# Optimization experiments

Measured on AMD Instinct MI355X. Metric: run time of the kernel, lower is better.

## Reference

```python
import jax, jax.numpy as jnp
import numpy as np

N_NODES = 50000
N_EDGES = 800000
N_POS = 200000
NFEAT = 512
NHID = 256


def setup_inputs() -> dict:
    key = jax.random.key(0)
    ks = jax.random.split(key, 7)
    x = jax.random.normal(ks[0], (N_NODES, NFEAT), dtype=jnp.float32)
    edge_index = jax.random.randint(ks[1], (2, N_EDGES), 0, N_NODES, dtype=jnp.int32)
    edge_weight = jax.random.uniform(ks[2], (N_EDGES,), dtype=jnp.float32)
    pos_edge_index = jax.random.randint(ks[3], (2, N_POS), 0, N_NODES, dtype=jnp.int32)
    W1 = jax.random.normal(ks[4], (NFEAT, NHID), dtype=jnp.float32) * (1.0 / np.sqrt(NFEAT))
    W2 = jax.random.normal(ks[5], (NHID, NHID), dtype=jnp.float32) * (1.0 / np.sqrt(NHID))
    Wlin = jax.random.normal(ks[6], (2 * NHID, 2), dtype=jnp.float32) * (1.0 / np.sqrt(2 * NHID))
    return {"x": x, "edge_index": edge_index, "edge_weight": edge_weight,
            "pos_edge_index": pos_edge_index, "W1": W1, "W2": W2, "Wlin": Wlin}


def _gcn_conv(h, W, src, dst, edge_weight, num_nodes):
    # GCNConv(normalize=False, add_self_loops=False, bias=False):
    # out[dst] += edge_weight * (h @ W)[src]
    h = h @ W  # [N, out]
    msg = edge_weight[:, None] * h[src]  # [E, out]
    return jax.ops.segment_sum(msg, dst, num_segments=num_nodes)


def reference(x, edge_index, edge_weight, pos_edge_index, W1, W2, Wlin):
    src, dst = edge_index[0], edge_index[1]
    n = x.shape[0]
    z = _gcn_conv(x, W1, src, dst, edge_weight, n)
    z = jax.nn.relu(z)
    z = _gcn_conv(z, W2, src, dst, edge_weight, n)
    # decode: gather endpoints, concat, linear (no bias)
    h = jnp.concatenate([z[pos_edge_index[0]], z[pos_edge_index[1]]], axis=1)  # [P, 2*nhid]
    return h @ Wlin  # [P, 2]
```

## Files before the change

### kernel.cpp

```cpp
#include <hip/hip_runtime.h>

#define NHID 256
#define NFEAT 512

using short8  = __attribute__((ext_vector_type(8))) short;
using float8  = __attribute__((ext_vector_type(8))) float;
using f32x4   = __attribute__((ext_vector_type(4))) float;

__device__ __forceinline__ float b2f(unsigned short u) {
    union { float f; unsigned v; } c;
    c.v = ((unsigned)u) << 16;
    return c.f;
}
__device__ __forceinline__ unsigned short f2b(float f) {
    union { float f; unsigned u; } c;
    c.f = f;
    unsigned r = c.u + 0x7fffu + ((c.u >> 16) & 1u);
    return (unsigned short)(r >> 16);
}
__device__ __forceinline__ unsigned short f2h(float f) {
    union { _Float16 h; unsigned short u; } c;
    c.h = (_Float16)f;
    return c.u;
}
__device__ __forceinline__ float h2f(unsigned short u) {
    union { _Float16 h; unsigned short u; } c;
    c.u = u;
    return (float)c.h;
}

__device__ __forceinline__ void gload16(const void* gsrc, void* lds) {
    __builtin_amdgcn_global_load_lds((const __attribute__((address_space(1))) unsigned int*)gsrc,
                                     (__attribute__((address_space(3))) unsigned int*)lds,
                                     16, 0, 0);
}

__global__ __launch_bounds__(256) void prep_all(const float* __restrict__ W1,
                                                const float* __restrict__ W2,
                                                const float* __restrict__ Wlin,
                                                unsigned short* __restrict__ F1,
                                                float* __restrict__ WP,
                                                int* __restrict__ cursor, int M) {
    int i = blockIdx.x * blockDim.x + threadIdx.x;
    const int T1 = NFEAT * NHID;
    if (i < T1) {
        int j = i & 7, l = (i >> 3) & 63, cb = (i >> 9) & 15, t = i >> 13;
        int n = cb * 16 + (l & 15);
        int k = t * 32 + ((l >> 4) << 3) + j;
        F1[i] = f2b(W1[k * NHID + n]);
    } else if (i < T1 + NHID * 4) {
        int i3 = i - T1;
        int k = i3 >> 2, j = i3 & 3;
        const int base = (j >= 2) ? NHID : 0;
        const int col = j & 1;
        float acc = 0.f;
        for (int n = 0; n < NHID; ++n)
            acc += W2[k * NHID + n] * Wlin[(base + n) * 2 + col];
        WP[k * 4 + j] = acc;
    } else {
        int j = i - T1 - NHID * 4;
        if (j < M) cursor[j] = 0;
    }
}

__device__ __forceinline__ void gemm1_body(const float* __restrict__ x,
                                           const unsigned short* __restrict__ F1,
                                           unsigned short* __restrict__ C, int M,
                                           int brow, char* AsRaw ) {
    const int tid = threadIdx.x;
    const int lane = tid & 63;
    const int wc = tid >> 6;
    const int lrow = lane & 15;
    const int lq = lane >> 4;
    const int nt = NFEAT / 32;

    int ar0 = brow + wc * 16 + (lane >> 3);
    int ar1 = ar0 + 8;
    if (ar0 >= M) ar0 = M - 1;
    if (ar1 >= M) ar1 = M - 1;
    const int aswz = ((lane & 7) ^ (lane >> 3)) * 4;
    const float* ag0 = x + (size_t)ar0 * NFEAT + aswz;
    const float* ag1 = x + (size_t)ar1 * NFEAT + aswz;
    const unsigned short* bsrc = F1 + (wc * 4) * 512 + lane * 8;

    f32x4 acc[4][4] = {};

    gload16(ag0, AsRaw + wc * 2048);
    gload16(ag1, AsRaw + wc * 2048 + 1024);
    short8 bc0 = *(const short8*)(bsrc + 0 * 512);
    short8 bc1 = *(const short8*)(bsrc + 1 * 512);
    short8 bc2 = *(const short8*)(bsrc + 2 * 512);
    short8 bc3 = *(const short8*)(bsrc + 3 * 512);
    __syncthreads();

    int p = 0;
#pragma unroll
    for (int t = 0; t < 16; ++t) {
        short8 bn0, bn1, bn2, bn3;
        if (t + 1 < nt) {
            gload16(ag0 + (t + 1) * 32, AsRaw + (p ^ 1) * 8192 + wc * 2048);
            gload16(ag1 + (t + 1) * 32, AsRaw + (p ^ 1) * 8192 + wc * 2048 + 1024);
            const unsigned short* bs_ = bsrc + (t + 1) * 8192;
            bn0 = *(const short8*)(bs_ + 0 * 512);
            bn1 = *(const short8*)(bs_ + 1 * 512);
            bn2 = *(const short8*)(bs_ + 2 * 512);
            bn3 = *(const short8*)(bs_ + 3 * 512);
        }
        short8 a[4];
#pragma unroll
        for (int m = 0; m < 4; ++m) {
            int row = m * 16 + lrow;
            const char* base = AsRaw + p * 8192 + row * 128;
            int sw = (row & 7) << 4;
            float4 f0 = *(const float4*)(base + ((lq * 32) ^ sw));
            float4 f1 = *(const float4*)(base + ((lq * 32 + 16) ^ sw));
            short8 v;
            v[0] = (short)f2b(f0.x); v[1] = (short)f2b(f0.y);
            v[2] = (short)f2b(f0.z); v[3] = (short)f2b(f0.w);
            v[4] = (short)f2b(f1.x); v[5] = (short)f2b(f1.y);
            v[6] = (short)f2b(f1.z); v[7] = (short)f2b(f1.w);
            a[m] = v;
        }
#pragma unroll
        for (int m = 0; m < 4; ++m) {
            acc[m][0] = __builtin_amdgcn_mfma_f32_16x16x32_bf16(a[m], bc0, acc[m][0], 0, 0, 0);
            acc[m][1] = __builtin_amdgcn_mfma_f32_16x16x32_bf16(a[m], bc1, acc[m][1], 0, 0, 0);
            acc[m][2] = __builtin_amdgcn_mfma_f32_16x16x32_bf16(a[m], bc2, acc[m][2], 0, 0, 0);
            acc[m][3] = __builtin_amdgcn_mfma_f32_16x16x32_bf16(a[m], bc3, acc[m][3], 0, 0, 0);
        }
        __syncthreads();
        p ^= 1;
        bc0 = bn0; bc1 = bn1; bc2 = bn2; bc3 = bn3;
    }

#pragma unroll
    for (int m = 0; m < 4; ++m)
#pragma unroll
        for (int r = 0; r < 4; ++r) {
            int row = brow + m * 16 + (lane >> 4) * 4 + r;
            if (row < M) {
#pragma unroll
                for (int n = 0; n < 4; ++n) {
                    int col = wc * 64 + n * 16 + (lane & 15);
                    C[(size_t)row * NHID + col] = f2b(acc[m][n][r]);
                }
            }
        }
}

__global__ __launch_bounds__(256) void fused_g1_histrank(const float* __restrict__ x,
                                                         const unsigned short* __restrict__ F1,
                                                         unsigned short* __restrict__ C, int M,
                                                         int gblocks,
                                                         const int* __restrict__ dst,
                                                         int* __restrict__ counts,
                                                         int* __restrict__ rank, int E) {
    __shared__ char AsRaw[2 * 8192];
    if ((int)blockIdx.x < gblocks) {
        gemm1_body(x, F1, C, M, blockIdx.x * 64, AsRaw);
    } else {
        const int rank_b = blockIdx.x - gblocks;
        const int nrank = gridDim.x - gblocks;
        for (int e = rank_b * blockDim.x + threadIdx.x; e < E; e += nrank * blockDim.x)
            rank[e] = atomicAdd(&counts[dst[e]], 1);
    }
}

__global__ __launch_bounds__(256) void fused_g1_ranksort(const float* __restrict__ x,
                                                         const unsigned short* __restrict__ F1,
                                                         unsigned short* __restrict__ C, int M,
                                                         int gblocks, int rowbase,
                                                         const int* __restrict__ src,
                                                         const int* __restrict__ dst,
                                                         const float* __restrict__ w,
                                                         const int* __restrict__ offsets,
                                                         const int* __restrict__ rank,
                                                         unsigned* __restrict__ pk,
                                                         int E, int span) {
    __shared__ char AsRaw[2 * 8192];
    if ((int)blockIdx.x < gblocks) {
        gemm1_body(x, F1, C, M, (rowbase + blockIdx.x) * 64, AsRaw);
    } else {
        const int rb = blockIdx.x - gblocks;
        const int nrb = gridDim.x - gblocks;
        const int g = rb & 7;
        const int r8 = rb >> 3;
        const int n8 = nrb >> 3;
        const int lo = g * span;
        const int hi = min(lo + span, M);
        for (int e = r8 * blockDim.x + threadIdx.x; e < E; e += n8 * blockDim.x) {
            int d = dst[e];
            if (d >= lo && d < hi)
                pk[offsets[d] + rank[e]] = ((unsigned)f2h(w[e]) << 16) | (unsigned)src[e];
        }
    }
}

__global__ __launch_bounds__(1024) void scan_local(const int* __restrict__ counts,
                                                   int* __restrict__ local,
                                                   int* __restrict__ blocksums, int n) {
    __shared__ int s[1024];
    const int tid = threadIdx.x;
    const int idx = blockIdx.x * 1024 + tid;
    int v = (idx < n) ? counts[idx] : 0;
    s[tid] = v;
    __syncthreads();
    for (int off = 1; off < 1024; off <<= 1) {
        int t = (tid >= off) ? s[tid - off] : 0;
        __syncthreads();
        s[tid] += t;
        __syncthreads();
    }
    if (idx < n) local[idx] = s[tid] - v;
    if (tid == 1023) blocksums[blockIdx.x] = s[1023];
}

__global__ __launch_bounds__(1024) void scan_sums(int* __restrict__ blocksums, int nb) {
    __shared__ int s[1024];
    const int tid = threadIdx.x;
    int v = (tid < nb) ? blocksums[tid] : 0;
    s[tid] = v;
    __syncthreads();
    for (int off = 1; off < 1024; off <<= 1) {
        int t = (tid >= off) ? s[tid - off] : 0;
        __syncthreads();
        s[tid] += t;
        __syncthreads();
    }
    if (tid < nb) blocksums[tid] = s[tid] - v;
}

__global__ __launch_bounds__(256) void scan_finalize(int* __restrict__ offsets,
                                                     const int* __restrict__ blockoffs,
                                                     int n, int total) {
    int idx = blockIdx.x * blockDim.x + threadIdx.x;
    if (idx < n) offsets[idx] += blockoffs[idx >> 10];
    if (idx == 0) offsets[n] = total;
}

__global__ __launch_bounds__(256) void gather1_proj(const unsigned short* __restrict__ h,
                                                    const int* __restrict__ offsets,
                                                    const unsigned* __restrict__ pk,
                                                    const float* __restrict__ WP,
                                                    float4* __restrict__ y4, int N) {
    const int lane = threadIdx.x & 63;
    const int wid = threadIdx.x >> 6;
    const int node = blockIdx.x * 4 + wid;
    if (node >= N) return;

    float wp[4][4];
#pragma unroll
    for (int i = 0; i < 4; ++i) {
        float4 r = ((const float4*)WP)[lane * 4 + i];
        wp[i][0] = r.x; wp[i][1] = r.y; wp[i][2] = r.z; wp[i][3] = r.w;
    }

    const int s0 = offsets[node];
    const int s1 = offsets[node + 1];
    float a0 = 0.f, a1 = 0.f, a2 = 0.f, a3 = 0.f;
    int i = s0;
    for (; i + 4 <= s1; i += 4) {
        unsigned qA = pk[i], qB = pk[i + 1], qC = pk[i + 2], qD = pk[i + 3];
        float wA = h2f(qA >> 16), wB = h2f(qB >> 16), wC = h2f(qC >> 16), wD = h2f(qD >> 16);
        ushort4 vA = ((const ushort4*)(h + (size_t)(qA & 0xffffu) * NHID))[lane];
        ushort4 vB = ((const ushort4*)(h + (size_t)(qB & 0xffffu) * NHID))[lane];
        ushort4 vC = ((const ushort4*)(h + (size_t)(qC & 0xffffu) * NHID))[lane];
        ushort4 vD = ((const ushort4*)(h + (size_t)(qD & 0xffffu) * NHID))[lane];
        a0 += wA * b2f(vA.x) + wB * b2f(vB.x) + wC * b2f(vC.x) + wD * b2f(vD.x);
        a1 += wA * b2f(vA.y) + wB * b2f(vB.y) + wC * b2f(vC.y) + wD * b2f(vD.y);
        a2 += wA * b2f(vA.z) + wB * b2f(vB.z) + wC * b2f(vC.z) + wD * b2f(vD.z);
        a3 += wA * b2f(vA.w) + wB * b2f(vB.w) + wC * b2f(vC.w) + wD * b2f(vD.w);
    }
    for (; i < s1; ++i) {
        unsigned q = pk[i];
        float ww = h2f(q >> 16);
        ushort4 v = ((const ushort4*)(h + (size_t)(q & 0xffffu) * NHID))[lane];
        a0 += ww * b2f(v.x);
        a1 += ww * b2f(v.y);
        a2 += ww * b2f(v.z);
        a3 += ww * b2f(v.w);
    }
    a0 = fmaxf(a0, 0.f); a1 = fmaxf(a1, 0.f);
    a2 = fmaxf(a2, 0.f); a3 = fmaxf(a3, 0.f);

    float t0 = a0 * wp[0][0] + a1 * wp[1][0] + a2 * wp[2][0] + a3 * wp[3][0];
    float t1 = a0 * wp[0][1] + a1 * wp[1][1] + a2 * wp[2][1] + a3 * wp[3][1];
    float t2 = a0 * wp[0][2] + a1 * wp[1][2] + a2 * wp[2][2] + a3 * wp[3][2];
    float t3 = a0 * wp[0][3] + a1 * wp[1][3] + a2 * wp[2][3] + a3 * wp[3][3];
#pragma unroll
    for (int off = 32; off > 0; off >>= 1) {
        t0 += __shfl_down(t0, off);
        t1 += __shfl_down(t1, off);
        t2 += __shfl_down(t2, off);
        t3 += __shfl_down(t3, off);
    }
    if (lane == 0) y4[node] = {t0, t1, t2, t3};
}

__global__ __launch_bounds__(256) void gather2_small(const float4* __restrict__ y4,
                                                     const int* __restrict__ offsets,
                                                     const unsigned* __restrict__ pk,
                                                     float2* __restrict__ za,
                                                     float2* __restrict__ zb, int N) {
    const int lane = threadIdx.x & 63;
    const int wid = threadIdx.x >> 6;
    const int grp = lane >> 4;
    const int slot = lane & 15;
    const int node = blockIdx.x * 16 + wid * 4 + grp;
    if (node >= N) return;

    const int s0 = offsets[node];
    const int s1 = offsets[node + 1];
    float x0 = 0.f, x1 = 0.f, x2 = 0.f, x3 = 0.f;
    for (int i = s0 + slot; i < s1; i += 16) {
        unsigned q = pk[i];
        float ww = h2f(q >> 16);
        float4 v = y4[q & 0xffffu];
        x0 += ww * v.x; x1 += ww * v.y; x2 += ww * v.z; x3 += ww * v.w;
    }
#pragma unroll
    for (int off = 8; off > 0; off >>= 1) {
        x0 += __shfl_xor(x0, off);
        x1 += __shfl_xor(x1, off);
        x2 += __shfl_xor(x2, off);
        x3 += __shfl_xor(x3, off);
    }
    if (slot == 0) {
        za[node] = {x0, x1};
        zb[node] = {x2, x3};
    }
}

__global__ __launch_bounds__(256) void decode_pairs(const float2* __restrict__ za,
                                                    const float2* __restrict__ zb,
                                                    const int* __restrict__ ps,
                                                    const int* __restrict__ pd,
                                                    float2* __restrict__ out, int P) {
    int p = blockIdx.x * blockDim.x + threadIdx.x;
    if (p < P) {
        float2 va = za[ps[p]];
        float2 vb = zb[pd[p]];
        out[p] = {va.x + vb.x, va.y + vb.y};
    }
}

template <bool RELU>
__global__ __launch_bounds__(256) void gemm_tiled(const float* __restrict__ A,
                                                  const float* __restrict__ B,
                                                  float* __restrict__ C,
                                                  int M, int N, int K) {
    __shared__ float As[16][65];
    __shared__ float Bs[16][64];
    const int block_row = blockIdx.x * 64;
    const int block_col = blockIdx.y * 64;
    const int tid = threadIdx.x;
    const int tx = tid & 15;
    const int ty = tid >> 4;
    float c[4][4] = {};
    for (int k0 = 0; k0 < K; k0 += 16) {
#pragma unroll
        for (int i = 0; i < 4; ++i) {
            int idx = tid + i * 256;
            int kk = idx & 15;
            int m = idx >> 4;
            int row = block_row + m;
            float v = 0.f;
            if (row < M) v = A[(long)row * K + k0 + kk];
            if (RELU) v = fmaxf(v, 0.f);
            As[kk][m] = v;
        }
#pragma unroll
        for (int i = 0; i < 4; ++i) {
            int idx = tid + i * 256;
            int n = idx & 63;
            int kk = idx >> 6;
            Bs[kk][n] = B[(long)(k0 + kk) * N + block_col + n];
        }
        __syncthreads();
#pragma unroll
        for (int kk = 0; kk < 16; ++kk) {
            float a[4], b[4];
#pragma unroll
            for (int i = 0; i < 4; ++i) a[i] = As[kk][ty * 4 + i];
#pragma unroll
            for (int j = 0; j < 4; ++j) b[j] = Bs[kk][tx * 4 + j];
#pragma unroll
            for (int i = 0; i < 4; ++i)
#pragma unroll
                for (int j = 0; j < 4; ++j) c[i][j] += a[i] * b[j];
        }
        __syncthreads();
    }
#pragma unroll
    for (int i = 0; i < 4; ++i) {
        int row = block_row + ty * 4 + i;
        if (row < M) {
            float* cp = C + (long)row * N + block_col + tx * 4;
#pragma unroll
            for (int j = 0; j < 4; ++j) cp[j] = c[i][j];
        }
    }
}

__global__ __launch_bounds__(256) void scatter_conv(const float* __restrict__ h,
                                                    const int* __restrict__ src,
                                                    const int* __restrict__ dst,
                                                    const float* __restrict__ w,
                                                    float* __restrict__ z, int E) {
    const int lane = threadIdx.x & 63;
    const int wid = threadIdx.x >> 6;
    const int nwaves = (gridDim.x * blockDim.x) >> 6;
    for (int e = blockIdx.x * 4 + wid; e < E; e += nwaves) {
        int s = src[e];
        int d = dst[e];
        float ww = w[e];
        float4 v = ((const float4*)(h + (long)s * NHID))[lane];
        float* zp = z + (long)d * NHID + lane * 4;
        atomicAdd(zp + 0, ww * v.x);
        atomicAdd(zp + 1, ww * v.y);
        atomicAdd(zp + 2, ww * v.z);
        atomicAdd(zp + 3, ww * v.w);
    }
}

__global__ __launch_bounds__(256) void decode_f(const float* __restrict__ z,
                                                const int* __restrict__ ps,
                                                const int* __restrict__ pd,
                                                const float* __restrict__ Wlin,
                                                float* __restrict__ out, int P) {
    const int lane = threadIdx.x & 63;
    const int wid = threadIdx.x >> 6;
    const int nwaves = (gridDim.x * blockDim.x) >> 6;
    float wa[8], wb[8];
#pragma unroll
    for (int i = 0; i < 8; ++i) {
        wa[i] = Wlin[(lane * 4) * 2 + i];
        wb[i] = Wlin[(NHID + lane * 4) * 2 + i];
    }
    for (int p = blockIdx.x * 4 + wid; p < P; p += nwaves) {
        int a = ps[p];
        int b = pd[p];
        float4 va = ((const float4*)(z + (long)a * NHID))[lane];
        float4 vb = ((const float4*)(z + (long)b * NHID))[lane];
        float acc0 = va.x * wa[0] + va.y * wa[2] + va.z * wa[4] + va.w * wa[6]
                   + vb.x * wb[0] + vb.y * wb[2] + vb.z * wb[4] + vb.w * wb[6];
        float acc1 = va.x * wa[1] + va.y * wa[3] + va.z * wa[5] + va.w * wa[7]
                   + vb.x * wb[1] + vb.y * wb[3] + vb.z * wb[5] + vb.w * wb[7];
#pragma unroll
        for (int off = 32; off > 0; off >>= 1) {
            acc0 += __shfl_down(acc0, off);
            acc1 += __shfl_down(acc1, off);
        }
        if (lane == 0) {
            out[(long)p * 2 + 0] = acc0;
            out[(long)p * 2 + 1] = acc1;
        }
    }
}

extern "C" void kernel_launch(void* const* d_in, const int* in_sizes, int n_in,
                              void* d_out, int out_size, void* d_ws, size_t ws_size,
                              hipStream_t stream) {
    (void)n_in; (void)out_size;
    const float* x    = (const float*)d_in[0];
    const int*   ei   = (const int*)d_in[1];
    const float* ew   = (const float*)d_in[2];
    const int*   pei  = (const int*)d_in[3];
    const float* W1   = (const float*)d_in[4];
    const float* W2   = (const float*)d_in[5];
    const float* Wlin = (const float*)d_in[6];
    float* out = (float*)d_out;

    const int E = in_sizes[2];
    const int P = in_sizes[3] / 2;
    const int M = in_sizes[0] / NFEAT;

    dim3 blk(256);
    const int* src = ei;
    const int* dst = ei + E;

    unsigned short* hA = (unsigned short*)d_ws;
    unsigned short* hB = hA + (size_t)M * NHID;
    int* offsets = (int*)(hB + (size_t)M * NHID);
    int* cursor  = offsets + (M + 1);
    unsigned* pk = (unsigned*)(cursor + M);
    int* rank    = (int*)(pk + E);
    int* blocksums = rank + E;
    float2* za = (float2*)(blocksums + 1024);
    float2* zb = za + M;
    const size_t need = 2 * (size_t)M * NHID * 2 + ((size_t)2 * M + 1) * 4
                      + (size_t)E * 8 + 1024 * 4 + (size_t)M * 2 * 8;

    if (ws_size >= need && M <= 65535) {
        unsigned short* F1 = (unsigned short*)d_out;
        float* WP = (float*)((char*)d_out + (size_t)NFEAT * NHID * 2);
        float4* y4 = (float4*)hB;

        const int span = (M + 7) / 8;
        const int nb = (M + 1023) / 1024;
        const int g = (M + 63) / 64;
        const int g1 = g / 2;
        const int g2 = g - g1;
        const int CSRB = 1024;

        const int zt = NFEAT * NHID + NHID * 4 + M;
        prep_all<<<(zt + 255) / 256, blk, 0, stream>>>(W1, W2, Wlin, F1, WP, cursor, M);

        fused_g1_histrank<<<g1 + CSRB, blk, 0, stream>>>(x, F1, hA, M, g1, dst, cursor, rank, E);
        scan_local<<<nb, 1024, 0, stream>>>(cursor, offsets, blocksums, M);
        scan_sums<<<1, 1024, 0, stream>>>(blocksums, nb);
        scan_finalize<<<(M + 255) / 256, blk, 0, stream>>>(offsets, blocksums, M, E);
        fused_g1_ranksort<<<g2 + CSRB, blk, 0, stream>>>(x, F1, hA, M, g2, g1,
                                                         src, dst, ew, offsets, rank, pk, E, span);
        gather1_proj<<<(M + 3) / 4, blk, 0, stream>>>(hA, offsets, pk, WP, y4, M);
        gather2_small<<<(M + 15) / 16, blk, 0, stream>>>(y4, offsets, pk, za, zb, M);
        decode_pairs<<<(P + 255) / 256, blk, 0, stream>>>(za, zb, pei, pei + P, (float2*)out, P);
    } else {
        float* bufA = (float*)d_ws;
        float* bufB = bufA + (size_t)M * NHID;
        const size_t zbytes = (size_t)M * NHID * sizeof(float);
        dim3 gemm_grid((M + 63) / 64, NHID / 64);
        gemm_tiled<false><<<gemm_grid, blk, 0, stream>>>(x, W1, bufA, M, NHID, NFEAT);
        hipMemsetAsync(bufB, 0, zbytes, stream);
        scatter_conv<<<2048, blk, 0, stream>>>(bufA, src, dst, ew, bufB, E);
        gemm_tiled<true><<<gemm_grid, blk, 0, stream>>>(bufB, W2, bufA, M, NHID, NHID);
        hipMemsetAsync(bufB, 0, zbytes, stream);
        scatter_conv<<<2048, blk, 0, stream>>>(bufA, src, dst, ew, bufB, E);
        decode_f<<<(P + 3) / 4, blk, 0, stream>>>(bufB, pei, pei + P, Wlin, out, P);
    }
}
```

Baseline: 176.9 us.

## Fuse weight prep with histogram ranking and run full GEMM1 alongside CSR sort

Histogram/rank atomics now share a launch with the weight-prep work, with a memset zeroing the counters. All GEMM1 row blocks then run in a single launch together with the rank-sort scatter, where before they were split across two launches. This drops the GEMM1 launch that overlapped the histogram and reorganizes the overlap. The risk is that GEMM1 no longer overlaps the histogram pass, so the ranksort launch carries the whole GEMM. The hi bound change to M+1 looks harmless.

```diff
diff --git a/kernel.cpp b/kernel.cpp
--- a/kernel.cpp
+++ b/kernel.cpp
@@ -35,31 +35,38 @@
                                      16, 0, 0);
 }
 
-__global__ __launch_bounds__(256) void prep_all(const float* __restrict__ W1,
-                                                const float* __restrict__ W2,
-                                                const float* __restrict__ Wlin,
-                                                unsigned short* __restrict__ F1,
-                                                float* __restrict__ WP,
-                                                int* __restrict__ cursor, int M) {
-    int i = blockIdx.x * blockDim.x + threadIdx.x;
-    const int T1 = NFEAT * NHID;
-    if (i < T1) {
-        int j = i & 7, l = (i >> 3) & 63, cb = (i >> 9) & 15, t = i >> 13;
-        int n = cb * 16 + (l & 15);
-        int k = t * 32 + ((l >> 4) << 3) + j;
-        F1[i] = f2b(W1[k * NHID + n]);
-    } else if (i < T1 + NHID * 4) {
-        int i3 = i - T1;
-        int k = i3 >> 2, j = i3 & 3;
-        const int base = (j >= 2) ? NHID : 0;
-        const int col = j & 1;
-        float acc = 0.f;
-        for (int n = 0; n < NHID; ++n)
-            acc += W2[k * NHID + n] * Wlin[(base + n) * 2 + col];
-        WP[k * 4 + j] = acc;
+__global__ __launch_bounds__(256) void fused_prep_histrank(const float* __restrict__ W1,
+                                                           const float* __restrict__ W2,
+                                                           const float* __restrict__ Wlin,
+                                                           unsigned short* __restrict__ F1,
+                                                           float* __restrict__ WP,
+                                                           int prepb,
+                                                           const int* __restrict__ dst,
+                                                           int* __restrict__ counts,
+                                                           int* __restrict__ rank, int E) {
+    if ((int)blockIdx.x < prepb) {
+        int i = blockIdx.x * blockDim.x + threadIdx.x;
+        const int T1 = NFEAT * NHID;
+        if (i < T1) {
+            int j = i & 7, l = (i >> 3) & 63, cb = (i >> 9) & 15, t = i >> 13;
+            int n = cb * 16 + (l & 15);
+            int k = t * 32 + ((l >> 4) << 3) + j;
+            F1[i] = f2b(W1[k * NHID + n]);
+        } else if (i < T1 + NHID * 4) {
+            int i3 = i - T1;
+            int k = i3 >> 2, j = i3 & 3;
+            const int base = (j >= 2) ? NHID : 0;
+            const int col = j & 1;
+            float acc = 0.f;
+            for (int n = 0; n < NHID; ++n)
+                acc += W2[k * NHID + n] * Wlin[(base + n) * 2 + col];
+            WP[k * 4 + j] = acc;
+        }
     } else {
-        int j = i - T1 - NHID * 4;
-        if (j < M) cursor[j] = 0;
+        const int rank_b = blockIdx.x - prepb;
+        const int nrank = gridDim.x - prepb;
+        for (int e = rank_b * blockDim.x + threadIdx.x; e < E; e += nrank * blockDim.x)
+            rank[e] = atomicAdd(&counts[dst[e]], 1);
     }
 }
 
@@ -148,28 +155,10 @@
         }
 }
 
-__global__ __launch_bounds__(256) void fused_g1_histrank(const float* __restrict__ x,
+__global__ __launch_bounds__(256) void fused_g1_ranksort(const float* __restrict__ x,
                                                          const unsigned short* __restrict__ F1,
                                                          unsigned short* __restrict__ C, int M,
                                                          int gblocks,
-                                                         const int* __restrict__ dst,
-                                                         int* __restrict__ counts,
-                                                         int* __restrict__ rank, int E) {
-    __shared__ char AsRaw[2 * 8192];
-    if ((int)blockIdx.x < gblocks) {
-        gemm1_body(x, F1, C, M, blockIdx.x * 64, AsRaw);
-    } else {
-        const int rank_b = blockIdx.x - gblocks;
-        const int nrank = gridDim.x - gblocks;
-        for (int e = rank_b * blockDim.x + threadIdx.x; e < E; e += nrank * blockDim.x)
-            rank[e] = atomicAdd(&counts[dst[e]], 1);
-    }
-}
-
-__global__ __launch_bounds__(256) void fused_g1_ranksort(const float* __restrict__ x,
-                                                         const unsigned short* __restrict__ F1,
-                                                         unsigned short* __restrict__ C, int M,
-                                                         int gblocks, int rowbase,
                                                          const int* __restrict__ src,
                                                          const int* __restrict__ dst,
                                                          const float* __restrict__ w,
@@ -179,7 +168,7 @@
                                                          int E, int span) {
     __shared__ char AsRaw[2 * 8192];
     if ((int)blockIdx.x < gblocks) {
-        gemm1_body(x, F1, C, M, (rowbase + blockIdx.x) * 64, AsRaw);
+        gemm1_body(x, F1, C, M, blockIdx.x * 64, AsRaw);
     } else {
         const int rb = blockIdx.x - gblocks;
         const int nrb = gridDim.x - gblocks;
@@ -187,7 +176,7 @@
         const int r8 = rb >> 3;
         const int n8 = nrb >> 3;
         const int lo = g * span;
-        const int hi = min(lo + span, M);
+        const int hi = min(lo + span, M + 1);
         for (int e = r8 * blockDim.x + threadIdx.x; e < E; e += n8 * blockDim.x) {
             int d = dst[e];
             if (d >= lo && d < hi)
@@ -499,19 +488,16 @@
         const int span = (M + 7) / 8;
         const int nb = (M + 1023) / 1024;
         const int g = (M + 63) / 64;
-        const int g1 = g / 2;
-        const int g2 = g - g1;
-        const int CSRB = 1024;
-
-        const int zt = NFEAT * NHID + NHID * 4 + M;
-        prep_all<<<(zt + 255) / 256, blk, 0, stream>>>(W1, W2, Wlin, F1, WP, cursor, M);
-
-        fused_g1_histrank<<<g1 + CSRB, blk, 0, stream>>>(x, F1, hA, M, g1, dst, cursor, rank, E);
+        const int prepb = (NFEAT * NHID + NHID * 4 + 255) / 256;
+
+        hipMemsetAsync(cursor, 0, (size_t)M * sizeof(int), stream);
+        fused_prep_histrank<<<prepb + 1024, blk, 0, stream>>>(W1, W2, Wlin, F1, WP, prepb,
+                                                              dst, cursor, rank, E);
         scan_local<<<nb, 1024, 0, stream>>>(cursor, offsets, blocksums, M);
         scan_sums<<<1, 1024, 0, stream>>>(blocksums, nb);
         scan_finalize<<<(M + 255) / 256, blk, 0, stream>>>(offsets, blocksums, M, E);
-        fused_g1_ranksort<<<g2 + CSRB, blk, 0, stream>>>(x, F1, hA, M, g2, g1,
-                                                         src, dst, ew, offsets, rank, pk, E, span);
+        fused_g1_ranksort<<<g + 1024, blk, 0, stream>>>(x, F1, hA, M, g,
+                                                        src, dst, ew, offsets, rank, pk, E, span);
         gather1_proj<<<(M + 3) / 4, blk, 0, stream>>>(hA, offsets, pk, WP, y4, M);
         gather2_small<<<(M + 15) / 16, blk, 0, stream>>>(y4, offsets, pk, za, zb, M);
         decode_pairs<<<(P + 255) / 256, blk, 0, stream>>>(za, zb, pei, pei + P, (float2*)out, P);
```

After: 189.2 us. 7.0% more time.
